# Kernel optimization log

Hardware: AMD Instinct MI355X
Metric: run time of the kernel (lower is better)

The kernel has to match this reference:

```python
import jax, jax.numpy as jnp
import numpy as np

E = 1152          # embed_dim (Qwen3-VL vision hidden_size)
H = 16            # num_heads
D = E // H        # head_dim = 72
SEG = 8           # number of frames / attention segments
HW = 32           # each frame is 32x32 patches -> seg_len = 1024
L = HW * HW
S = SEG * L       # total tokens = 8192


def _make_rotary(S):
    # VisionRotaryEmbedding(dim=head_dim//2): inv_freq over arange(0, 36, 2)/36 -> 18 freqs
    half = D // 2  # 36
    inv_freq = 1.0 / (10000.0 ** (jnp.arange(0, half, 2, dtype=jnp.float32) / half))  # (18,)
    # 2D (h,w) position ids within each 32x32 frame, tiled across frames
    hpos = jnp.tile(jnp.repeat(jnp.arange(HW, dtype=jnp.float32), HW), SEG)  # (S,)
    wpos = jnp.tile(jnp.tile(jnp.arange(HW, dtype=jnp.float32), HW), SEG)    # (S,)
    fh = hpos[:, None] * inv_freq[None, :]   # (S, 18)
    fw = wpos[:, None] * inv_freq[None, :]   # (S, 18)
    freqs = jnp.concatenate([fh, fw], axis=-1)       # (S, 36)
    emb = jnp.concatenate([freqs, freqs], axis=-1)   # (S, 72) = head_dim
    return jnp.cos(emb), jnp.sin(emb)


def setup_inputs() -> dict:
    key = jax.random.key(0)
    k = jax.random.split(key, 6)
    std = 1.0 / np.sqrt(E)
    cos, sin = _make_rotary(S)
    return {
        "x": jax.random.normal(k[0], (S, E), jnp.float32),
        "cos": cos,
        "sin": sin,
        "qkv_w": jax.random.normal(k[1], (3 * E, E), jnp.float32) * std,
        "qkv_b": jax.random.normal(k[2], (3 * E,), jnp.float32) * 0.02,
        "proj_w": jax.random.normal(k[3], (E, E), jnp.float32) * std,
        "proj_b": jax.random.normal(k[4], (E,), jnp.float32) * 0.02,
        "cu_seqlens": jnp.arange(SEG + 1, dtype=jnp.int32) * L,
    }


def _rope(t, cos, sin):
    # t: (S, H, D); cos/sin: (S, D) broadcast over heads (matches cos.unsqueeze(1))
    half = t.shape[-1] // 2
    t1, t2 = t[..., :half], t[..., half:]
    rot = jnp.concatenate([-t2, t1], axis=-1)
    return t * cos[:, None, :] + rot * sin[:, None, :]


def reference(x, cos, sin, qkv_w, qkv_b, proj_w, proj_b, cu_seqlens):
    S_, E_ = x.shape
    qkv = x @ qkv_w.T + qkv_b                     # (S, 3E)
    q, k, v = jnp.split(qkv, 3, axis=-1)
    q = _rope(q.reshape(S_, H, D), cos, sin)
    k = _rope(k.reshape(S_, H, D), cos, sin)
    v = v.reshape(S_, H, D)
    # Equal-length segments (one per frame): block-diagonal attention via reshape,
    # honoring cu_seqlens structure without materializing an (S, S) mask.
    nseg = cu_seqlens.shape[0] - 1
    Lseg = S_ // nseg
    qs = q.reshape(nseg, Lseg, H, D)
    ks = k.reshape(nseg, Lseg, H, D)
    vs = v.reshape(nseg, Lseg, H, D)
    scale = 1.0 / np.sqrt(D)
    logits = jnp.einsum('gqhd,gkhd->ghqk', qs, ks) * scale   # (nseg, H, L, L)
    attn = jax.nn.softmax(logits, axis=-1)
    out = jnp.einsum('ghqk,gkhd->gqhd', attn, vs).reshape(S_, E_)
    return out @ proj_w.T + proj_b
```

## Files before the change

kernel.cpp:

```cpp
#include <hip/hip_runtime.h>
#include <hip/hip_bf16.h>
#include <stdint.h>

#define SEGN 8
#define LSEG 1024
#define SS   8192
#define EE   1152
#define HH   16
#define DD   72
#define DP   96
#define E3   3456
#define E3P  3584
#define EEP  1280

typedef __attribute__((ext_vector_type(8)))  __bf16 bf16x8;
typedef __attribute__((ext_vector_type(4)))  float  f32x4;
typedef __attribute__((ext_vector_type(16))) float  f32x16;
typedef __attribute__((ext_vector_type(4)))  unsigned int u32x4;

__device__ __forceinline__ short f2b(float x) {
  __hip_bfloat16 h = __float2bfloat16(x);
  return __builtin_bit_cast(short, h);
}
__device__ __forceinline__ float b2f(short x) {
  return __bfloat162float(__builtin_bit_cast(__hip_bfloat16, x));
}
__device__ __forceinline__ unsigned int pk2(float x, float y) {
  return (unsigned int)(unsigned short)f2b(x) |
         ((unsigned int)(unsigned short)f2b(y) << 16);
}
__device__ __forceinline__ void gload16(const void* g, void* l) {
  __builtin_amdgcn_global_load_lds(
      (const __attribute__((address_space(1))) unsigned int*)g,
      (__attribute__((address_space(3))) unsigned int*)l, 16, 0, 0);
}

#define BAR() __builtin_amdgcn_s_barrier()

__global__ void k_cvt(const float* __restrict__ in, short* __restrict__ out, int n4) {
  int i = blockIdx.x * blockDim.x + threadIdx.x;
  int stride = gridDim.x * blockDim.x;
  for (; i < n4; i += stride) {
    float4 v = reinterpret_cast<const float4*>(in)[i];
    short4 o;
    o.x = f2b(v.x); o.y = f2b(v.y); o.z = f2b(v.z); o.w = f2b(v.w);
    reinterpret_cast<short4*>(out)[i] = o;
  }
}

template <int OUT_BF16>
__global__ __launch_bounds__(512, 2) void k_gemm256(
    const short* __restrict__ A, const short* __restrict__ B,
    const float* __restrict__ bias, void* __restrict__ Cout,
    int K, int Nreal)
{
  __shared__ __align__(16) short Als[2][4][64 * 64];
  __shared__ __align__(16) short Bls[2][4][64 * 64];
  const int t = threadIdx.x;
  const int lane = t & 63, wave = t >> 6;
  const int r16 = lane & 15, kg = lane >> 4;
  const int wm = wave >> 2, wn = wave & 3;
  const int m0 = blockIdx.x * 256, n0 = blockIdx.y * 256;
  const int NT = K >> 6;

  const int D = t * 16;
  const int L = D ^ (((D >> 7) & 7) << 4);
  const int srow = L >> 7, scol = (L & 127) >> 1;
  const short* pa = A + (size_t)(m0 + srow) * K + scol;
  const short* pb = B + (size_t)(n0 + srow) * K + scol;
  const int K64 = K * 64;

#define STAGE_A(bf, h, kt_) do { \
    gload16(pa + (h) * K64 + (kt_) * 64, (char*)Als[bf][h] + D); \
    gload16(pa + ((h) + 2) * K64 + (kt_) * 64, (char*)Als[bf][(h) + 2] + D); } while (0)
#define STAGE_B(bf, h, kt_) do { \
    gload16(pb + (h) * K64 + (kt_) * 64, (char*)Bls[bf][h] + D); \
    gload16(pb + ((h) + 2) * K64 + (kt_) * 64, (char*)Bls[bf][(h) + 2] + D); } while (0)

  const int cA0 = (kg * 16) ^ ((r16 & 7) << 4);
  const int cA1 = (64 + kg * 16) ^ ((r16 & 7) << 4);

  f32x4 acc[8][4] = {};

  STAGE_A(0, 0, 0); STAGE_B(0, 0, 0);
  STAGE_A(0, 1, 0); STAGE_B(0, 1, 0);
  STAGE_A(1, 0, 1); STAGE_B(1, 0, 1);
  asm volatile("s_waitcnt vmcnt(4)" ::: "memory");
  BAR();

  for (int kt = 0; kt < NT; ++kt) {
    const int bsel = kt & 1, bn1 = bsel ^ 1;
    const bool s1 = (kt + 1 < NT), s2 = (kt + 2 < NT);
    const char* aq0 = (const char*)Als[bsel][2 * wm];
    const char* aq1 = (const char*)Als[bsel][2 * wm + 1];
    const char* bq  = (const char*)Bls[bsel][wn];

    bf16x8 a_[2][2], b_[4][2];

#pragma unroll
    for (int mi = 0; mi < 2; ++mi) {
      a_[mi][0] = *(const bf16x8*)(aq0 + (mi * 16 + r16) * 128 + cA0);
      a_[mi][1] = *(const bf16x8*)(aq0 + (mi * 16 + r16) * 128 + cA1);
    }
#pragma unroll
    for (int n = 0; n < 4; ++n) {
      b_[n][0] = *(const bf16x8*)(bq + (n * 16 + r16) * 128 + cA0);
      b_[n][1] = *(const bf16x8*)(bq + (n * 16 + r16) * 128 + cA1);
    }
    if (s1) STAGE_A(bn1, 1, kt + 1);
    BAR();
    __builtin_amdgcn_s_setprio(1);
#pragma unroll
    for (int mi = 0; mi < 2; ++mi)
#pragma unroll
      for (int n = 0; n < 4; ++n) {
        acc[mi][n] = __builtin_amdgcn_mfma_f32_16x16x32_bf16(a_[mi][0], b_[n][0], acc[mi][n], 0, 0, 0);
        acc[mi][n] = __builtin_amdgcn_mfma_f32_16x16x32_bf16(a_[mi][1], b_[n][1], acc[mi][n], 0, 0, 0);
      }
    __builtin_amdgcn_s_setprio(0);
    BAR();

#pragma unroll
    for (int mi = 0; mi < 2; ++mi) {
      a_[mi][0] = *(const bf16x8*)(aq0 + ((mi + 2) * 16 + r16) * 128 + cA0);
      a_[mi][1] = *(const bf16x8*)(aq0 + ((mi + 2) * 16 + r16) * 128 + cA1);
    }
    if (s1) STAGE_B(bn1, 1, kt + 1);
    BAR();
    __builtin_amdgcn_s_setprio(1);
#pragma unroll
    for (int mi = 0; mi < 2; ++mi)
#pragma unroll
      for (int n = 0; n < 4; ++n) {
        acc[mi + 2][n] = __builtin_amdgcn_mfma_f32_16x16x32_bf16(a_[mi][0], b_[n][0], acc[mi + 2][n], 0, 0, 0);
        acc[mi + 2][n] = __builtin_amdgcn_mfma_f32_16x16x32_bf16(a_[mi][1], b_[n][1], acc[mi + 2][n], 0, 0, 0);
      }
    __builtin_amdgcn_s_setprio(0);
    BAR();

#pragma unroll
    for (int mi = 0; mi < 2; ++mi) {
      a_[mi][0] = *(const bf16x8*)(aq1 + (mi * 16 + r16) * 128 + cA0);
      a_[mi][1] = *(const bf16x8*)(aq1 + (mi * 16 + r16) * 128 + cA1);
    }
    if (s2) STAGE_A(bsel, 0, kt + 2);
    BAR();
    __builtin_amdgcn_s_setprio(1);
#pragma unroll
    for (int mi = 0; mi < 2; ++mi)
#pragma unroll
      for (int n = 0; n < 4; ++n) {
        acc[mi + 4][n] = __builtin_amdgcn_mfma_f32_16x16x32_bf16(a_[mi][0], b_[n][0], acc[mi + 4][n], 0, 0, 0);
        acc[mi + 4][n] = __builtin_amdgcn_mfma_f32_16x16x32_bf16(a_[mi][1], b_[n][1], acc[mi + 4][n], 0, 0, 0);
      }
    __builtin_amdgcn_s_setprio(0);
    BAR();

#pragma unroll
    for (int mi = 0; mi < 2; ++mi) {
      a_[mi][0] = *(const bf16x8*)(aq1 + ((mi + 2) * 16 + r16) * 128 + cA0);
      a_[mi][1] = *(const bf16x8*)(aq1 + ((mi + 2) * 16 + r16) * 128 + cA1);
    }
    if (s2) STAGE_B(bsel, 0, kt + 2);
    BAR();
    __builtin_amdgcn_s_setprio(1);
#pragma unroll
    for (int mi = 0; mi < 2; ++mi)
#pragma unroll
      for (int n = 0; n < 4; ++n) {
        acc[mi + 6][n] = __builtin_amdgcn_mfma_f32_16x16x32_bf16(a_[mi][0], b_[n][0], acc[mi + 6][n], 0, 0, 0);
        acc[mi + 6][n] = __builtin_amdgcn_mfma_f32_16x16x32_bf16(a_[mi][1], b_[n][1], acc[mi + 6][n], 0, 0, 0);
      }
    __builtin_amdgcn_s_setprio(0);
    if (s2) { asm volatile("s_waitcnt vmcnt(4)" ::: "memory"); }
    else    { asm volatile("s_waitcnt vmcnt(0)" ::: "memory"); }
    BAR();
  }
#undef STAGE_A
#undef STAGE_B

#pragma unroll
  for (int n = 0; n < 4; ++n) {
    int col = n0 + wn * 64 + n * 16 + r16;
    if (col < Nreal) {
      float bv = bias[col];
#pragma unroll
      for (int m = 0; m < 8; ++m)
#pragma unroll
        for (int r = 0; r < 4; ++r) {
          int row = m0 + wm * 128 + m * 16 + kg * 4 + r;
          float v = acc[m][n][r] + bv;
          if (OUT_BF16) ((short*)Cout)[(size_t)row * Nreal + col] = f2b(v);
          else          ((float*)Cout)[(size_t)row * Nreal + col] = v;
        }
    }
  }
}

__global__ __launch_bounds__(256) void k_rope(
    const short* __restrict__ qkv, const float* __restrict__ cosb, const float* __restrict__ sinb,
    short* __restrict__ Qg, short* __restrict__ Kg, short* __restrict__ Vg)
{
  __shared__ short vt[72][64];
  const int b = blockIdx.x;
  const int seg = b >> 8, head = (b >> 4) & 15, pb = b & 15;
  const int pos0 = pb * 64;
  const int t = threadIdx.x;
  const int sh = seg * 16 + head;
  const float qscale = 0.17002540410995343f;

#pragma unroll
  for (int i = 0; i < 24; ++i) {
    int e = t + i * 256;
    int p = e / 96, d = e % 96;
    int s = seg * 1024 + pos0 + p;
    int ob = (sh * 1024 + pos0 + p) * 96 + d;
    short qo = 0, ko = 0;
    if (d < 72) {
      int base = s * E3 + head * 72;
      float c = cosb[s * 72 + d], sn = sinb[s * 72 + d];
      int d2 = d < 36 ? d + 36 : d - 36;
      float sgn = d < 36 ? -1.f : 1.f;
      float q1 = b2f(qkv[base + d]),        q2 = b2f(qkv[base + d2]);
      float k1 = b2f(qkv[base + 1152 + d]), k2 = b2f(qkv[base + 1152 + d2]);
      qo = f2b((q1 * c + sgn * q2 * sn) * qscale);
      ko = f2b(k1 * c + sgn * k2 * sn);
    }
    Qg[ob] = qo;
    Kg[ob] = ko;
  }
  for (int i = 0; i < 18; ++i) {
    int e = t + i * 256;
    int p = e / 72, d = e % 72;
    int s = seg * 1024 + pos0 + p;
    vt[d][p] = qkv[s * E3 + 2304 + head * 72 + d];
  }
  __syncthreads();
#pragma unroll
  for (int i = 0; i < 24; ++i) {
    int e = t + i * 256;
    int d = e >> 6, p = e & 63;
    short v;
    if (d < 72)       v = vt[d][p];
    else if (d == 72) v = (short)0x3F80;
    else              v = 0;
    Vg[(sh * 96 + d) * 1024 + pos0 + p] = v;
  }
}

#define KSS 104
#define VTS 72
__global__ __launch_bounds__(256, 2) void k_attn(
    const short* __restrict__ Qg, const short* __restrict__ Kg, const short* __restrict__ Vg,
    short* __restrict__ Og)
{
  __shared__ __align__(16) short Ks[2][64 * KSS];
  __shared__ __align__(16) short VT[2][96 * VTS];
  const int p_ = blockIdx.x;
  const int xcd = p_ & 7, rest = p_ >> 3;
  const int qb = rest & 7, shi = rest >> 3;
  const int sh = xcd * 16 + shi;
  const int seg = sh >> 4, head = sh & 15;
  const int t = threadIdx.x, lane = t & 63, wave = t >> 6;
  const int l31 = lane & 31, hi = lane >> 5;
  const int q0 = qb * 128 + wave * 32;

  bf16x8 qf[5];
  {
    const short* qp = Qg + ((size_t)(sh * 1024 + q0 + l31)) * 96 + hi * 8;
#pragma unroll
    for (int dm = 0; dm < 5; ++dm) qf[dm] = *(const bf16x8*)(qp + dm * 16);
  }

  const short* kbase = Kg + (size_t)sh * 1024 * 96;
  const short* vbase = Vg + (size_t)sh * 96 * 1024;
  int koff[4], voff[4];
#pragma unroll
  for (int i = 0; i < 4; ++i) {
    int c = t + i * 256;
    int kr = c / 13, kc8 = c - kr * 13;
    koff[i] = kr * 96 + ((kc8 == 12) ? 0 : kc8 * 8);
    int vr = c / 9, vc8 = c - vr * 9;
    voff[i] = vr * 1024 + ((vc8 == 8) ? 0 : vc8 * 8);
  }

  f32x16 acc0 = {}, acc1 = {}, acc2 = {};
  float Mrun = -1e30f;

  {
    const short* kp = kbase;
    const short* vp = vbase;
#pragma unroll
    for (int i = 0; i < 3; ++i) {
      gload16(kp + koff[i], (char*)Ks[0] + (t + i * 256) * 16);
      gload16(vp + voff[i], (char*)VT[0] + (t + i * 256) * 16);
    }
    if (t < 64) gload16(kp + koff[3], (char*)Ks[0] + (t + 768) * 16);
    if (t < 96) gload16(vp + voff[3], (char*)VT[0] + (t + 768) * 16);
  }
  __syncthreads();

  for (int kt = 0; kt < 16; ++kt) {
    const int cur = kt & 1;
    if (kt < 15) {
      const int nb = cur ^ 1;
      const short* kp = kbase + (kt + 1) * 64 * 96;
      const short* vp = vbase + (kt + 1) * 64;
#pragma unroll
      for (int i = 0; i < 3; ++i) {
        gload16(kp + koff[i], (char*)Ks[nb] + (t + i * 256) * 16);
        gload16(vp + voff[i], (char*)VT[nb] + (t + i * 256) * 16);
      }
      if (t < 64) gload16(kp + koff[3], (char*)Ks[nb] + (t + 768) * 16);
      if (t < 96) gload16(vp + voff[3], (char*)VT[nb] + (t + 768) * 16);
    }

    f32x16 s0 = {}, s1 = {};
    __builtin_amdgcn_s_setprio(1);
#pragma unroll
    for (int dm = 0; dm < 5; ++dm) {
      bf16x8 kf0 = *(const bf16x8*)&Ks[cur][l31 * KSS + dm * 16 + hi * 8];
      bf16x8 kf1 = *(const bf16x8*)&Ks[cur][(32 + l31) * KSS + dm * 16 + hi * 8];
      s0 = __builtin_amdgcn_mfma_f32_32x32x16_bf16(kf0, qf[dm], s0, 0, 0, 0);
      s1 = __builtin_amdgcn_mfma_f32_32x32x16_bf16(kf1, qf[dm], s1, 0, 0, 0);
    }
    __builtin_amdgcn_s_setprio(0);

    float pmax = s0[0];
#pragma unroll
    for (int r = 1; r < 16; ++r) pmax = fmaxf(pmax, s0[r]);
#pragma unroll
    for (int r = 0; r < 16; ++r) pmax = fmaxf(pmax, s1[r]);
    pmax = fmaxf(pmax, __shfl_xor(pmax, 32));

    if (__any(pmax > Mrun + 8.0f)) {
      float mn = fmaxf(Mrun, pmax);
      float corr = exp2f(Mrun - mn);
      Mrun = mn;
#pragma unroll
      for (int r = 0; r < 16; ++r) {
        int qr = (r & 3) + 8 * (r >> 2) + 4 * hi;
        float cr = __shfl(corr, qr);
        acc0[r] *= cr; acc1[r] *= cr; acc2[r] *= cr;
      }
    }

    unsigned int pk0[8], pk1[8];
#pragma unroll
    for (int b = 0; b < 4; ++b)
#pragma unroll
      for (int i = 0; i < 2; ++i) {
        pk0[b * 2 + i] = pk2(exp2f(s0[b * 4 + 2 * i] - Mrun), exp2f(s0[b * 4 + 2 * i + 1] - Mrun));
        pk1[b * 2 + i] = pk2(exp2f(s1[b * 4 + 2 * i] - Mrun), exp2f(s1[b * 4 + 2 * i + 1] - Mrun));
      }

    __builtin_amdgcn_s_setprio(1);
#pragma unroll
    for (int ks = 0; ks < 4; ++ks) {
      const int k1 = ks & 1;
      unsigned int A0, A1, B0, B1;
      if (ks < 2) { A0 = pk0[4 * k1]; A1 = pk0[4 * k1 + 1]; B0 = pk0[4 * k1 + 2]; B1 = pk0[4 * k1 + 3]; }
      else        { A0 = pk1[4 * k1]; A1 = pk1[4 * k1 + 1]; B0 = pk1[4 * k1 + 2]; B1 = pk1[4 * k1 + 3]; }
      unsigned int SA0 = __shfl_xor((int)A0, 32), SA1 = __shfl_xor((int)A1, 32);
      unsigned int SB0 = __shfl_xor((int)B0, 32), SB1 = __shfl_xor((int)B1, 32);
      u32x4 wv;
      wv.x = hi ? SB0 : A0;
      wv.y = hi ? SB1 : A1;
      wv.z = hi ? B0 : SA0;
      wv.w = hi ? B1 : SA1;
      bf16x8 af = __builtin_bit_cast(bf16x8, wv);
      bf16x8 vf0 = *(const bf16x8*)&VT[cur][l31 * VTS + ks * 16 + hi * 8];
      bf16x8 vf1 = *(const bf16x8*)&VT[cur][(32 + l31) * VTS + ks * 16 + hi * 8];
      bf16x8 vf2 = *(const bf16x8*)&VT[cur][(64 + l31) * VTS + ks * 16 + hi * 8];
      acc0 = __builtin_amdgcn_mfma_f32_32x32x16_bf16(af, vf0, acc0, 0, 0, 0);
      acc1 = __builtin_amdgcn_mfma_f32_32x32x16_bf16(af, vf1, acc1, 0, 0, 0);
      acc2 = __builtin_amdgcn_mfma_f32_32x32x16_bf16(af, vf2, acc2, 0, 0, 0);
    }
    __builtin_amdgcn_s_setprio(0);

    __syncthreads();
  }

#pragma unroll
  for (int r = 0; r < 16; ++r) {
    float l = __shfl(acc2[r], (lane & 32) | 8);
    float inv = 1.0f / l;
    int q = q0 + (r & 3) + 8 * (r >> 2) + 4 * hi;
    size_t base = (size_t)(seg * 1024 + q) * 1152 + head * 72;
    Og[base + l31]      = f2b(acc0[r] * inv);
    Og[base + 32 + l31] = f2b(acc1[r] * inv);
    if (l31 < 8) Og[base + 64 + l31] = f2b(acc2[r] * inv);
  }
}

extern "C" void kernel_launch(void* const* d_in, const int* in_sizes, int n_in,
                              void* d_out, int out_size, void* d_ws, size_t ws_size,
                              hipStream_t stream) {
  (void)in_sizes; (void)n_in; (void)out_size; (void)ws_size;
  const float* x      = (const float*)d_in[0];
  const float* cosb   = (const float*)d_in[1];
  const float* sinb   = (const float*)d_in[2];
  const float* qkv_w  = (const float*)d_in[3];
  const float* qkv_b  = (const float*)d_in[4];
  const float* proj_w = (const float*)d_in[5];
  const float* proj_b = (const float*)d_in[6];

  char* ws = (char*)d_ws;
  size_t o = 0;
  short* xb  = (short*)(ws + o); o += (size_t)SS * EE * 2;
  short* qwb = (short*)(ws + o); o += (size_t)E3P * EE * 2;
  short* pwb = (short*)(ws + o); o += (size_t)EEP * EE * 2;
  short* qkv = (short*)(ws + o); o += (size_t)SS * E3 * 2;
  short* Qg  = (short*)(ws + o); o += (size_t)SEGN * HH * LSEG * DP * 2;
  short* Kg  = (short*)(ws + o); o += (size_t)SEGN * HH * LSEG * DP * 2;
  short* Vg  = (short*)(ws + o); o += (size_t)SEGN * HH * DP * LSEG * 2;
  short* og  = xb;

  k_cvt<<<2048, 256, 0, stream>>>(x, xb, SS * EE / 4);
  k_cvt<<<1024, 256, 0, stream>>>(qkv_w, qwb, E3 * EE / 4);
  k_cvt<<<512, 256, 0, stream>>>(proj_w, pwb, EE * EE / 4);

  dim3 g1(SS / 256, E3P / 256);
  k_gemm256<1><<<g1, 512, 0, stream>>>(xb, qwb, qkv_b, qkv, EE, E3);

  k_rope<<<SEGN * HH * 16, 256, 0, stream>>>(qkv, cosb, sinb, Qg, Kg, Vg);

  k_attn<<<SEGN * HH * 8, 256, 0, stream>>>(Qg, Kg, Vg, og);

  dim3 g2(SS / 256, EEP / 256);
  k_gemm256<0><<<g2, 512, 0, stream>>>(og, pwb, proj_b, d_out, EE, EE);
}
```

Baseline: 264.8 us.

## Rewrite GEMM with fragment-major LDS layout, BK=32 staging, templated M tile

Replaces the 256x256 GEMM kernel with one that stages 32-wide K slices so each lane's 16-byte MFMA fragment sits contiguously in LDS, removing the XOR swizzle and the four barrier-separated sub-phases. A single double-buffered prefetch plus one __syncthreads per K step replaces the fine-grained vmcnt pipelining. The M tile is templated, and the output projection now uses 128-row tiles so more blocks fill the GPU. Risks: global loads are now 16 bytes strided across rows, which is less coalesced. Halving BK also doubles the number of barriers and loop iterations, and prefetch overlap is weaker.

New measurement: 331.4 us. 1.25x slower.

```diff
diff --git a/kernel.cpp b/kernel.cpp
--- a/kernel.cpp
+++ b/kernel.cpp
@@ -35,8 +35,6 @@
       (__attribute__((address_space(3))) unsigned int*)l, 16, 0, 0);
 }
 
-#define BAR() __builtin_amdgcn_s_barrier()
-
 __global__ void k_cvt(const float* __restrict__ in, short* __restrict__ out, int n4) {
   int i = blockIdx.x * blockDim.x + threadIdx.x;
   int stride = gridDim.x * blockDim.x;
@@ -48,136 +46,67 @@
   }
 }
 
-template <int OUT_BF16>
-__global__ __launch_bounds__(512, 2) void k_gemm256(
+template <int MFRAG, int OUT_BF16>
+__global__ __launch_bounds__(512, 2) void k_gemmf(
     const short* __restrict__ A, const short* __restrict__ B,
     const float* __restrict__ bias, void* __restrict__ Cout,
     int K, int Nreal)
 {
-  __shared__ __align__(16) short Als[2][4][64 * 64];
-  __shared__ __align__(16) short Bls[2][4][64 * 64];
+  constexpr int GA = MFRAG / 4;
+  __shared__ __align__(16) short Als[2][MFRAG * 1024];
+  __shared__ __align__(16) short Bls[2][8192];
   const int t = threadIdx.x;
-  const int lane = t & 63, wave = t >> 6;
+  const int lane = t & 63, w = t >> 6;
   const int r16 = lane & 15, kg = lane >> 4;
-  const int wm = wave >> 2, wn = wave & 3;
-  const int m0 = blockIdx.x * 256, n0 = blockIdx.y * 256;
-  const int NT = K >> 6;
-
-  const int D = t * 16;
-  const int L = D ^ (((D >> 7) & 7) << 4);
-  const int srow = L >> 7, scol = (L & 127) >> 1;
-  const short* pa = A + (size_t)(m0 + srow) * K + scol;
-  const short* pb = B + (size_t)(n0 + srow) * K + scol;
-  const int K64 = K * 64;
-
-#define STAGE_A(bf, h, kt_) do { \
-    gload16(pa + (h) * K64 + (kt_) * 64, (char*)Als[bf][h] + D); \
-    gload16(pa + ((h) + 2) * K64 + (kt_) * 64, (char*)Als[bf][(h) + 2] + D); } while (0)
-#define STAGE_B(bf, h, kt_) do { \
-    gload16(pb + (h) * K64 + (kt_) * 64, (char*)Bls[bf][h] + D); \
-    gload16(pb + ((h) + 2) * K64 + (kt_) * 64, (char*)Bls[bf][(h) + 2] + D); } while (0)
-
-  const int cA0 = (kg * 16) ^ ((r16 & 7) << 4);
-  const int cA1 = (64 + kg * 16) ^ ((r16 & 7) << 4);
-
-  f32x4 acc[8][4] = {};
-
-  STAGE_A(0, 0, 0); STAGE_B(0, 0, 0);
-  STAGE_A(0, 1, 0); STAGE_B(0, 1, 0);
-  STAGE_A(1, 0, 1); STAGE_B(1, 0, 1);
-  asm volatile("s_waitcnt vmcnt(4)" ::: "memory");
-  BAR();
+  const int wm = w >> 2, wn = w & 3;
+  const int m0 = blockIdx.x * (MFRAG * 32), n0 = blockIdx.y * 256;
+  const int NT = K >> 5;
+
+  const short* pa[2];
+  const short* pb[2];
+#pragma unroll
+  for (int g = 0; g < GA; ++g)
+    pa[g] = A + (size_t)(m0 + (g * 8 + w) * 16 + r16) * K + kg * 8;
+#pragma unroll
+  for (int g = 0; g < 2; ++g)
+    pb[g] = B + (size_t)(n0 + (g * 8 + w) * 16 + r16) * K + kg * 8;
+
+#define STAGEF(buf, kt_) do { \
+    _Pragma("unroll") \
+    for (int g = 0; g < GA; ++g) \
+      gload16(pa[g] + (kt_) * 32, (char*)Als[buf] + (g * 512 + w * 64) * 16); \
+    _Pragma("unroll") \
+    for (int g = 0; g < 2; ++g) \
+      gload16(pb[g] + (kt_) * 32, (char*)Bls[buf] + (g * 512 + w * 64) * 16); \
+  } while (0)
+
+  f32x4 acc[MFRAG][4] = {};
+
+  STAGEF(0, 0);
+  __syncthreads();
 
   for (int kt = 0; kt < NT; ++kt) {
-    const int bsel = kt & 1, bn1 = bsel ^ 1;
-    const bool s1 = (kt + 1 < NT), s2 = (kt + 2 < NT);
-    const char* aq0 = (const char*)Als[bsel][2 * wm];
-    const char* aq1 = (const char*)Als[bsel][2 * wm + 1];
-    const char* bq  = (const char*)Bls[bsel][wn];
-
-    bf16x8 a_[2][2], b_[4][2];
-
-#pragma unroll
-    for (int mi = 0; mi < 2; ++mi) {
-      a_[mi][0] = *(const bf16x8*)(aq0 + (mi * 16 + r16) * 128 + cA0);
-      a_[mi][1] = *(const bf16x8*)(aq0 + (mi * 16 + r16) * 128 + cA1);
-    }
-#pragma unroll
-    for (int n = 0; n < 4; ++n) {
-      b_[n][0] = *(const bf16x8*)(bq + (n * 16 + r16) * 128 + cA0);
-      b_[n][1] = *(const bf16x8*)(bq + (n * 16 + r16) * 128 + cA1);
-    }
-    if (s1) STAGE_A(bn1, 1, kt + 1);
-    BAR();
+    const int bsel = kt & 1;
+    if (kt + 1 < NT) STAGEF(bsel ^ 1, kt + 1);
+
+    const char* Ab = (const char*)Als[bsel] + (wm * MFRAG) * 1024 + lane * 16;
+    const char* Bb = (const char*)Bls[bsel] + (wn * 4) * 1024 + lane * 16;
+    bf16x8 b_[4];
+#pragma unroll
+    for (int n = 0; n < 4; ++n) b_[n] = *(const bf16x8*)(Bb + n * 1024);
     __builtin_amdgcn_s_setprio(1);
 #pragma unroll
-    for (int mi = 0; mi < 2; ++mi)
-#pragma unroll
-      for (int n = 0; n < 4; ++n) {
-        acc[mi][n] = __builtin_amdgcn_mfma_f32_16x16x32_bf16(a_[mi][0], b_[n][0], acc[mi][n], 0, 0, 0);
-        acc[mi][n] = __builtin_amdgcn_mfma_f32_16x16x32_bf16(a_[mi][1], b_[n][1], acc[mi][n], 0, 0, 0);
-      }
+    for (int mi = 0; mi < MFRAG; ++mi) {
+      bf16x8 a = *(const bf16x8*)(Ab + mi * 1024);
+#pragma unroll
+      for (int n = 0; n < 4; ++n)
+        acc[mi][n] = __builtin_amdgcn_mfma_f32_16x16x32_bf16(a, b_[n], acc[mi][n], 0, 0, 0);
+    }
     __builtin_amdgcn_s_setprio(0);
-    BAR();
-
-#pragma unroll
-    for (int mi = 0; mi < 2; ++mi) {
-      a_[mi][0] = *(const bf16x8*)(aq0 + ((mi + 2) * 16 + r16) * 128 + cA0);
-      a_[mi][1] = *(const bf16x8*)(aq0 + ((mi + 2) * 16 + r16) * 128 + cA1);
-    }
-    if (s1) STAGE_B(bn1, 1, kt + 1);
-    BAR();
-    __builtin_amdgcn_s_setprio(1);
-#pragma unroll
-    for (int mi = 0; mi < 2; ++mi)
-#pragma unroll
-      for (int n = 0; n < 4; ++n) {
-        acc[mi + 2][n] = __builtin_amdgcn_mfma_f32_16x16x32_bf16(a_[mi][0], b_[n][0], acc[mi + 2][n], 0, 0, 0);
-        acc[mi + 2][n] = __builtin_amdgcn_mfma_f32_16x16x32_bf16(a_[mi][1], b_[n][1], acc[mi + 2][n], 0, 0, 0);
-      }
-    __builtin_amdgcn_s_setprio(0);
-    BAR();
-
-#pragma unroll
-    for (int mi = 0; mi < 2; ++mi) {
-      a_[mi][0] = *(const bf16x8*)(aq1 + (mi * 16 + r16) * 128 + cA0);
-      a_[mi][1] = *(const bf16x8*)(aq1 + (mi * 16 + r16) * 128 + cA1);
-    }
-    if (s2) STAGE_A(bsel, 0, kt + 2);
-    BAR();
-    __builtin_amdgcn_s_setprio(1);
-#pragma unroll
-    for (int mi = 0; mi < 2; ++mi)
-#pragma unroll
-      for (int n = 0; n < 4; ++n) {
-        acc[mi + 4][n] = __builtin_amdgcn_mfma_f32_16x16x32_bf16(a_[mi][0], b_[n][0], acc[mi + 4][n], 0, 0, 0);
-        acc[mi + 4][n] = __builtin_amdgcn_mfma_f32_16x16x32_bf16(a_[mi][1], b_[n][1], acc[mi + 4][n], 0, 0, 0);
-      }
-    __builtin_amdgcn_s_setprio(0);
-    BAR();
-
-#pragma unroll
-    for (int mi = 0; mi < 2; ++mi) {
-      a_[mi][0] = *(const bf16x8*)(aq1 + ((mi + 2) * 16 + r16) * 128 + cA0);
-      a_[mi][1] = *(const bf16x8*)(aq1 + ((mi + 2) * 16 + r16) * 128 + cA1);
-    }
-    if (s2) STAGE_B(bsel, 0, kt + 2);
-    BAR();
-    __builtin_amdgcn_s_setprio(1);
-#pragma unroll
-    for (int mi = 0; mi < 2; ++mi)
-#pragma unroll
-      for (int n = 0; n < 4; ++n) {
-        acc[mi + 6][n] = __builtin_amdgcn_mfma_f32_16x16x32_bf16(a_[mi][0], b_[n][0], acc[mi + 6][n], 0, 0, 0);
-        acc[mi + 6][n] = __builtin_amdgcn_mfma_f32_16x16x32_bf16(a_[mi][1], b_[n][1], acc[mi + 6][n], 0, 0, 0);
-      }
-    __builtin_amdgcn_s_setprio(0);
-    if (s2) { asm volatile("s_waitcnt vmcnt(4)" ::: "memory"); }
-    else    { asm volatile("s_waitcnt vmcnt(0)" ::: "memory"); }
-    BAR();
-  }
-#undef STAGE_A
-#undef STAGE_B
+
+    __syncthreads();
+  }
+#undef STAGEF
 
 #pragma unroll
   for (int n = 0; n < 4; ++n) {
@@ -185,11 +114,11 @@
     if (col < Nreal) {
       float bv = bias[col];
 #pragma unroll
-      for (int m = 0; m < 8; ++m)
+      for (int mi = 0; mi < MFRAG; ++mi)
 #pragma unroll
         for (int r = 0; r < 4; ++r) {
-          int row = m0 + wm * 128 + m * 16 + kg * 4 + r;
-          float v = acc[m][n][r] + bv;
+          int row = m0 + (wm * MFRAG + mi) * 16 + kg * 4 + r;
+          float v = acc[mi][n][r] + bv;
           if (OUT_BF16) ((short*)Cout)[(size_t)row * Nreal + col] = f2b(v);
           else          ((float*)Cout)[(size_t)row * Nreal + col] = v;
         }
@@ -421,12 +350,12 @@
   k_cvt<<<512, 256, 0, stream>>>(proj_w, pwb, EE * EE / 4);
 
   dim3 g1(SS / 256, E3P / 256);
-  k_gemm256<1><<<g1, 512, 0, stream>>>(xb, qwb, qkv_b, qkv, EE, E3);
+  k_gemmf<8, 1><<<g1, 512, 0, stream>>>(xb, qwb, qkv_b, qkv, EE, E3);
 
   k_rope<<<SEGN * HH * 16, 256, 0, stream>>>(qkv, cosb, sinb, Qg, Kg, Vg);
 
   k_attn<<<SEGN * HH * 8, 256, 0, stream>>>(Qg, Kg, Vg, og);
 
-  dim3 g2(SS / 256, EEP / 256);
-  k_gemm256<0><<<g2, 512, 0, stream>>>(og, pwb, proj_b, d_out, EE, EE);
-}
+  dim3 g2(SS / 128, EEP / 256);
+  k_gemmf<4, 0><<<g2, 512, 0, stream>>>(og, pwb, proj_b, d_out, EE, EE);
+}
```
